# Kernel tuning notes

Measured on AMD Instinct MI355X. Metric: run time of the kernel, lower is better.

## Reference

```python
import jax, jax.numpy as jnp
import numpy as np

B, S, W = 32, 128, 16
E, CD, H, P = 256, 64, 512, 256
V, CV, NC = 50000, 256, 6
CK, WK = 8, 64  # merged char/word conv kernel sizes


def conv1d(x, w, b):
    # x: [N, Cin, L], w: [Cout, Cin, K] -> [N, Cout, L-K+1] (VALID)
    y = jax.lax.conv_general_dilated(x, w, (1,), 'VALID',
                                     dimension_numbers=('NCH', 'OIH', 'NCH'))
    return y + b[None, :, None]


def setup_inputs() -> dict:
    key = jax.random.key(0)
    ks = iter(jax.random.split(key, 40))
    nrm = lambda shape: jax.random.normal(next(ks), shape, dtype=jnp.float32) * 0.05
    return {
        'seq': jax.random.randint(next(ks), (B, S), 0, V),
        'seq_char': jax.random.randint(next(ks), (B, S, W), 0, CV),
        'classes': jnp.arange(NC, dtype=jnp.int32).reshape(NC, 1),
        'embed_w': nrm((V, E)),
        'char_embed_w': nrm((CV, CD)),
        'class_embed_w': nrm((NC, E)),
        'char_conv_w': nrm((CD, CD, CK)), 'char_conv_b': nrm((CD,)),
        'word_conv_w': nrm((E, E + CD, WK)), 'word_conv_b': nrm((E,)),
        'f_Wih': nrm((4 * H, E + CD)), 'f_Whh': nrm((4 * H, H)), 'f_b': nrm((4 * H,)),
        'b_Wih': nrm((4 * H, E + CD)), 'b_Whh': nrm((4 * H, H)), 'b_b': nrm((4 * H,)),
        'attend': nrm((E, 2 * H)),
        'd_Wih': nrm((6 * H, E + 2 * H)), 'd_Whh': nrm((6 * H, 2 * H)),
        'd_bih': nrm((6 * H,)), 'd_bhh': nrm((6 * H,)),
        'proj_w': nrm((P, 2 * H)), 'proj_b': nrm((P,)),
        'cls_w': nrm((2, P)), 'cls_b': nrm((2,)),
    }


def reference(seq, seq_char, classes, embed_w, char_embed_w, class_embed_w,
              char_conv_w, char_conv_b, word_conv_w, word_conv_b,
              f_Wih, f_Whh, f_b, b_Wih, b_Whh, b_b, attend,
              d_Wih, d_Whh, d_bih, d_bhh, proj_w, proj_b, cls_w, cls_b):
    # eval-mode forward (dropout p=0.01 is identity at eval time)
    Bq, Sq = seq.shape
    pad_mask = (seq > 0).astype(jnp.float32)            # [B,S]
    word_e = jnp.tanh(embed_w[seq])                     # [B,S,E]
    # char CNN: all char convs share kernel size -> merged into one conv
    ce = char_embed_w[seq_char]                         # [B,S,W,CD]
    ce = ce.reshape(Bq * Sq, W, CD).transpose(0, 2, 1)  # [B*S, CD, W]
    char_feat = jnp.tanh(conv1d(ce, char_conv_w, char_conv_b).mean(-1).reshape(Bq, Sq, CD))
    x = jnp.concatenate([word_e, char_feat], -1)        # [B,S,E+CD]
    # word CNN over full sequence -> [B,E]
    conv_seq = jnp.tanh(conv1d(x.transpose(0, 2, 1), word_conv_w, word_conv_b).mean(-1))
    # BiLSTM; backward direction uses seq_emb[-i], i.e. order [0, S-1, ..., 1] (as in original)
    xs = x.transpose(1, 0, 2)                           # [S,B,E+CD]
    xs_b = xs[(-jnp.arange(Sq)) % Sq]

    def lstm_scan(Wih, Whh, b, inputs):
        def step(carry, xt):
            h, c = carry
            g = xt @ Wih.T + h @ Whh.T + b
            i, f, gg, o = jnp.split(g, 4, axis=-1)
            c = jax.nn.sigmoid(f) * c + jax.nn.sigmoid(i) * jnp.tanh(gg)
            h = jax.nn.sigmoid(o) * jnp.tanh(c)
            return (h, c), h
        h0 = jnp.zeros((Bq, H), x.dtype)
        _, hs = jax.lax.scan(step, (h0, h0), inputs)
        return hs

    fouts = lstm_scan(f_Wih, f_Whh, f_b, xs)            # [S,B,H]
    bouts = lstm_scan(b_Wih, b_Whh, b_b, xs_b)[::-1]    # reversed, as in original
    seq_repr = jnp.concatenate([fouts, bouts], -1)      # [S,B,2H]
    h0 = seq_repr[-1]                                   # decoder init state [B,2H]
    seq_repr = seq_repr.transpose(1, 0, 2)              # [B,S,2H]
    # class attention: the expanded attn rows are identical across positions,
    # so sum over dim 1 of the [B,S,S] bmm equals S * tanh(a_c) . seq_repr[b,t]
    a = jnp.tanh(jnp.tanh(class_embed_w[classes[:, 0]])) @ attend   # [C,2H]
    scores = Sq * jnp.einsum('ch,bth->cbt', jnp.tanh(a), seq_repr)  # [C,B,S]
    scores = scores * pad_mask[None]
    att_ctx = jnp.einsum('cbt,bth->cbh', jnp.tanh(scores), seq_repr)  # [C,B,2H]

    def gru_step(h, ctx):
        inp = jnp.concatenate([conv_seq, ctx], -1)      # [B, E+2H]
        gi = inp @ d_Wih.T + d_bih
        gh = h @ d_Whh.T + d_bhh
        ir, iz, inn = jnp.split(gi, 3, -1)
        hr, hz, hn = jnp.split(gh, 3, -1)
        r = jax.nn.sigmoid(ir + hr)
        z = jax.nn.sigmoid(iz + hz)
        n = jnp.tanh(inn + r * hn)
        h_new = jnp.tanh((1 - z) * n + z * h)           # post-tanh state fed back (as in original)
        logits = (h_new @ proj_w.T + proj_b) @ cls_w.T + cls_b
        return h_new, jax.nn.log_softmax(logits, -1)

    _, outs = jax.lax.scan(gru_step, h0, att_ctx)       # [C,B,2]
    return outs
```

## Files before the change

kernel.cpp:

```cpp
#include <hip/hip_runtime.h>

typedef __bf16 bf16_t;
typedef __bf16 bf16x8 __attribute__((ext_vector_type(8)));
typedef float f32x4 __attribute__((ext_vector_type(4)));

static constexpr int BB = 32, SS = 128, WW = 16, EE = 256, CDm = 64, HH = 512, PP = 256;
static constexpr int EC = 320;
static constexpr int H2 = 1024;
static constexpr int G6 = 3072;
static constexpr int NKT = 28;
static constexpr int NKTX = 12;

__device__ __forceinline__ float sigm(float x){ return 1.f/(1.f + expf(-x)); }

__global__ void k_embed(const int* __restrict__ seq, const float* __restrict__ embed_w,
                        float* __restrict__ x, float* __restrict__ mask){
  int bs = blockIdx.x; int c = threadIdx.x;
  int wid = seq[bs];
  x[(size_t)bs*EC + c] = tanhf(embed_w[(size_t)wid*EE + c]);
  if (c == 0) mask[bs] = (wid > 0) ? 1.f : 0.f;
}

__global__ void k_cbar(const int* __restrict__ seq_char, const float* __restrict__ cemb,
                       float* __restrict__ cbar){
  int bs = blockIdx.x; int c = threadIdx.x;
  float ce[WW];
  #pragma unroll
  for (int p = 0; p < WW; ++p){
    int id = seq_char[bs*WW + p];
    ce[p] = cemb[(size_t)id*CDm + c];
  }
  #pragma unroll
  for (int k = 0; k < 8; ++k){
    float s = 0.f;
    #pragma unroll
    for (int p = 0; p < 9; ++p) s += ce[k+p];
    cbar[(size_t)bs*512 + c*8 + k] = s * (1.f/9.f);
  }
}

__global__ __launch_bounds__(64) void k_xbar(const float* __restrict__ x, float* __restrict__ xbar){
  __shared__ float xl[64][129];
  int gid = blockIdx.x*64 + threadIdx.x;
  int b = gid / EC, c = gid % EC;
  int tl = threadIdx.x;
  for (int t = 0; t < SS; ++t) xl[tl][t] = x[((size_t)b*SS + t)*EC + c];
  float s = 0.f;
  for (int t = 0; t < 65; ++t) s += xl[tl][t];
  const float inv = 1.f/65.f;
  float* o = &xbar[(size_t)(b*EC + c)*64];
  o[0] = s*inv;
  for (int k = 1; k < 64; ++k){ s += xl[tl][k+64] - xl[tl][k-1]; o[k] = s*inv; }
}

template<int BM,int BN,int TM,int TN>
__global__ __launch_bounds__(256) void k_gemm(const float* __restrict__ A,
    const float* __restrict__ Wm, float* __restrict__ part,
    int M, int N, int K, int kslice){
  __shared__ float As[32][BM+4];
  __shared__ float Ws[32][BN+4];
  const int tid = threadIdx.x;
  const int tx = tid & 15, ty = tid >> 4;
  const int m0 = blockIdx.x*BM, n0 = blockIdx.y*BN, ks = blockIdx.z;
  const int kb = ks*kslice;
  float acc[TM][TN];
  #pragma unroll
  for (int i = 0; i < TM; ++i)
    #pragma unroll
    for (int j = 0; j < TN; ++j) acc[i][j] = 0.f;
  for (int kt = 0; kt < kslice; kt += 32){
    constexpr int AIT = (BM*8)/256;
    #pragma unroll
    for (int it = 0; it < AIT; ++it){
      int ch = tid + it*256;
      int r = ch >> 3, kc = (ch & 7)*4;
      float4 v = *(const float4*)(A + (size_t)(m0+r)*K + kb + kt + kc);
      As[kc+0][r]=v.x; As[kc+1][r]=v.y; As[kc+2][r]=v.z; As[kc+3][r]=v.w;
    }
    constexpr int WIT = (BN*8)/256;
    #pragma unroll
    for (int it = 0; it < WIT; ++it){
      int ch = tid + it*256;
      int r = ch >> 3, kc = (ch & 7)*4;
      float4 v = *(const float4*)(Wm + (size_t)(n0+r)*K + kb + kt + kc);
      Ws[kc+0][r]=v.x; Ws[kc+1][r]=v.y; Ws[kc+2][r]=v.z; Ws[kc+3][r]=v.w;
    }
    __syncthreads();
    #pragma unroll
    for (int kk = 0; kk < 32; ++kk){
      float a[TM], wv[TN];
      #pragma unroll
      for (int i = 0; i < TM; ++i) a[i] = As[kk][ty*TM+i];
      #pragma unroll
      for (int j = 0; j < TN; ++j) wv[j] = Ws[kk][tx*TN+j];
      #pragma unroll
      for (int i = 0; i < TM; ++i)
        #pragma unroll
        for (int j = 0; j < TN; ++j) acc[i][j] = fmaf(a[i], wv[j], acc[i][j]);
    }
    __syncthreads();
  }
  #pragma unroll
  for (int i = 0; i < TM; ++i){
    int row = m0 + ty*TM + i;
    #pragma unroll
    for (int j = 0; j < TN; ++j){
      int col = n0 + tx*TN + j;
      part[((size_t)ks*M + row)*N + col] = acc[i][j];
    }
  }
}

__global__ __launch_bounds__(64) void k_fin(const float* __restrict__ part,
    const float* __restrict__ bias, float* __restrict__ out,
    int M, int N, int KS, int ldc, int act){
  int col = blockIdx.x*64 + threadIdx.x;
  int row = blockIdx.y;
  float v = bias ? bias[col] : 0.f;
  for (int ks = 0; ks < KS; ++ks) v += part[((size_t)ks*M + row)*N + col];
  if (act) v = tanhf(v);
  out[(size_t)row*ldc + col] = v;
}

__global__ __launch_bounds__(64) void k_packw(const float* __restrict__ fWih, const float* __restrict__ fWhh,
    const float* __restrict__ bWih, const float* __restrict__ bWhh, bf16_t* __restrict__ Wp){
  int id = blockIdx.x;
  int kt = id % NKT; id /= NKT;
  int slice = id % 32; int dir = id / 32;
  int l = threadIdx.x;
  const float* Whh = dir ? bWhh : fWhh;
  const float* Wih = dir ? bWih : fWih;
  int krow = (l >> 4)*8;
  for (int nt = 0; nt < 4; ++nt){
    int row = nt*512 + slice*16 + (l & 15);
    bf16_t* dst = &Wp[((((size_t)(dir*32+slice)*NKT + kt)*4 + nt)*64 + l)*8];
    if (kt < 16){
      const float* src = &Whh[(size_t)row*512 + kt*32 + krow];
      #pragma unroll
      for (int r = 0; r < 8; ++r) dst[r] = (bf16_t)src[r];
    } else {
      int kx = (kt-16)*32 + krow;
      if (kx + 8 <= 320){
        const float* src = &Wih[(size_t)row*320 + kx];
        #pragma unroll
        for (int r = 0; r < 8; ++r) dst[r] = (bf16_t)src[r];
      } else {
        #pragma unroll
        for (int r = 0; r < 8; ++r) dst[r] = (bf16_t)0.f;
      }
    }
  }
}

__global__ __launch_bounds__(64) void k_packdw(const float* __restrict__ W, bf16_t* __restrict__ Wo){
  int id = blockIdx.x;
  int kt = id % 32; id /= 32;
  int nt = id % 3;  int wg = id / 3;
  int l = threadIdx.x;
  int col = nt*1024 + wg*16 + (l & 15);
  int k0 = kt*32 + (l >> 4)*8;
  bf16_t* dst = Wo + (((size_t)(wg*3 + nt)*32 + kt)*64 + l)*8;
  const float* src = W + (size_t)col*1024 + k0;
  #pragma unroll
  for (int r = 0; r < 8; ++r) dst[r] = (bf16_t)src[r];
}

__global__ __launch_bounds__(64) void k_packpw(const float* __restrict__ W, bf16_t* __restrict__ Wo){
  int id = blockIdx.x;
  int kt = id & 31, wg = id >> 5;
  int l = threadIdx.x;
  int col = wg*16 + (l & 15);
  int k0 = kt*32 + (l >> 4)*8;
  bf16_t* dst = Wo + (((size_t)wg*32 + kt)*64 + l)*8;
  const float* src = W + (size_t)col*1024 + k0;
  #pragma unroll
  for (int r = 0; r < 8; ++r) dst[r] = (bf16_t)src[r];
}

__global__ __launch_bounds__(64) void k_packx(const float* __restrict__ x, bf16_t* __restrict__ xp){
  int id = blockIdx.x;
  int ktx = id % NKTX; id /= NKTX;
  int mt = id & 1; int t = id >> 1;
  int l = threadIdx.x;
  int b = (l & 15) + 16*mt;
  int c = ktx*32 + (l >> 4)*8;
  bf16_t* dst = &xp[(((size_t)t*2 + mt)*NKTX + ktx)*64*8 + (size_t)l*8];
  if (c + 8 <= EC){
    const float* src = &x[((size_t)b*SS + t)*EC + c];
    #pragma unroll
    for (int r = 0; r < 8; ++r) dst[r] = (bf16_t)src[r];
  } else {
    #pragma unroll
    for (int r = 0; r < 8; ++r) dst[r] = (bf16_t)0.f;
  }
}

__global__ __launch_bounds__(256) void k_zero(unsigned int* __restrict__ base){
  int i = blockIdx.x*256 + threadIdx.x;
  if (i < 35840) __hip_atomic_store(base + i, 0u, __ATOMIC_RELAXED, __HIP_MEMORY_SCOPE_AGENT);
}

__global__ __launch_bounds__(64) void k_hprep(const float* __restrict__ seq_repr, bf16_t* __restrict__ hdp){
  int mt = blockIdx.x >> 5, kt = blockIdx.x & 31, l = threadIdx.x;
  int b = mt*16 + (l & 15);
  int jb = kt*32 + (l >> 4)*8;
  const float* src = &seq_repr[((size_t)b*SS + 127)*H2 + jb];
  unsigned* dst = (unsigned*)(hdp + (((size_t)mt*32 + kt)*64 + l)*8);
  #pragma unroll
  for (int p = 0; p < 4; ++p){
    unsigned pk = (unsigned)__builtin_bit_cast(unsigned short, (bf16_t)src[2*p])
                | ((unsigned)__builtin_bit_cast(unsigned short, (bf16_t)src[2*p+1]) << 16);
    __hip_atomic_store(dst + p, pk, __ATOMIC_RELAXED, __HIP_MEMORY_SCOPE_AGENT);
  }
}

__global__ __launch_bounds__(256, 1) void k_lstm(const bf16_t* __restrict__ Wp,
    const bf16_t* __restrict__ xp, bf16_t* __restrict__ hp,
    const float* __restrict__ fb, const float* __restrict__ bb,
    float* __restrict__ seq_repr, unsigned int* __restrict__ lf){
  const int wg = blockIdx.x;
  const int dir = wg >> 5, slice = wg & 31;
  const int tid = threadIdx.x;
  const int wv = tid >> 6, lane = tid & 63;
  __shared__ __align__(16) bf16_t Wl[NKT*4*64*8];
  __shared__ float red[4][32][65];
  __shared__ float bias_l[64];
  __shared__ float c_l[16][32];
  {
    const uint4* src = (const uint4*)(Wp + ((size_t)(dir*32 + slice))*NKT*4*64*8);
    uint4* dst = (uint4*)Wl;
    for (int i = tid; i < NKT*4*64*8/8; i += 256) dst[i] = src[i];
  }
  if (tid < 64){
    const float* bv = dir ? bb : fb;
    bias_l[tid] = bv[(tid >> 4)*512 + slice*16 + (tid & 15)];
  }
  ((float*)c_l)[tid]       = 0.f;
  ((float*)c_l)[tid + 256] = 0.f;
  __syncthreads();

  union HU { unsigned long long u[2]; bf16x8 v; };

  for (int t = 0; t < SS; ++t){
    const int ph = t & 1;
    const int s = dir ? ((SS - t) & 127) : t;
    f32x4 acc[2][4];
    f32x4 zero = {0.f,0.f,0.f,0.f};
    #pragma unroll
    for (int m = 0; m < 2; ++m)
      #pragma unroll
      for (int n = 0; n < 4; ++n) acc[m][n] = zero;

    const bf16_t* xb = xp + (size_t)s*2*NKTX*64*8;
    bf16x8 ax[3][2];
    #pragma unroll
    for (int i = 0; i < 3; ++i){
      int ktx = wv*3 + i;
      #pragma unroll
      for (int m = 0; m < 2; ++m)
        ax[i][m] = *reinterpret_cast<const bf16x8*>(xb + (((size_t)m*NKTX + ktx)*64 + lane)*8);
    }
    #pragma unroll
    for (int i = 0; i < 3; ++i){
      int kt = 16 + wv*3 + i;
      #pragma unroll
      for (int nt = 0; nt < 4; ++nt){
        bf16x8 Bf = *reinterpret_cast<const bf16x8*>(&Wl[(((size_t)kt*4 + nt)*64 + lane)*8]);
        acc[0][nt] = __builtin_amdgcn_mfma_f32_16x16x32_bf16(ax[i][0], Bf, acc[0][nt], 0, 0, 0);
        acc[1][nt] = __builtin_amdgcn_mfma_f32_16x16x32_bf16(ax[i][1], Bf, acc[1][nt], 0, 0, 0);
      }
    }
    if (t > 0 && lane < 8){
      int prod = dir*32 + (wv + 4*(lane >> 1))*2 + (lane & 1);
      const unsigned int* fp = lf + prod*16;
      unsigned tgt = (unsigned)t;
      for(;;){
        unsigned v = __hip_atomic_load(fp, __ATOMIC_RELAXED, __HIP_MEMORY_SCOPE_AGENT);
        if (__ballot(v < tgt) == 0ull) break;
      }
    }
    const bf16_t* hb_ = hp + ((size_t)(ph*2 + dir))*2*16*64*8;
    bf16x8 ah[4][2];
    #pragma unroll
    for (int i = 0; i < 4; ++i){
      int kt = wv + 4*i;
      #pragma unroll
      for (int m = 0; m < 2; ++m){
        const unsigned long long* p =
            (const unsigned long long*)(hb_ + (((size_t)m*16 + kt)*64 + lane)*8);
        HU u;
        u.u[0] = __hip_atomic_load(p,     __ATOMIC_RELAXED, __HIP_MEMORY_SCOPE_AGENT);
        u.u[1] = __hip_atomic_load(p + 1, __ATOMIC_RELAXED, __HIP_MEMORY_SCOPE_AGENT);
        ah[i][m] = u.v;
      }
    }
    #pragma unroll
    for (int i = 0; i < 4; ++i){
      int kt = wv + 4*i;
      #pragma unroll
      for (int nt = 0; nt < 4; ++nt){
        bf16x8 Bf = *reinterpret_cast<const bf16x8*>(&Wl[(((size_t)kt*4 + nt)*64 + lane)*8]);
        acc[0][nt] = __builtin_amdgcn_mfma_f32_16x16x32_bf16(ah[i][0], Bf, acc[0][nt], 0, 0, 0);
        acc[1][nt] = __builtin_amdgcn_mfma_f32_16x16x32_bf16(ah[i][1], Bf, acc[1][nt], 0, 0, 0);
      }
    }
    {
      int r0 = (lane >> 4)*4, cc = lane & 15;
      #pragma unroll
      for (int m = 0; m < 2; ++m)
        #pragma unroll
        for (int n = 0; n < 4; ++n)
          #pragma unroll
          for (int e = 0; e < 4; ++e)
            red[wv][m*16 + r0 + e][n*16 + cc] = acc[m][n][e];
    }
    __syncthreads();
    {
      int b = tid & 31, jjp = tid >> 5;
      float hv[2];
      #pragma unroll
      for (int u2 = 0; u2 < 2; ++u2){
        int jj = jjp*2 + u2;
        float gi_ = bias_l[jj],     gf_ = bias_l[16+jj];
        float gg_ = bias_l[32+jj],  go_ = bias_l[48+jj];
        #pragma unroll
        for (int w2 = 0; w2 < 4; ++w2){
          gi_ += red[w2][b][jj];      gf_ += red[w2][b][16+jj];
          gg_ += red[w2][b][32+jj];   go_ += red[w2][b][48+jj];
        }
        float ii = sigm(gi_), ff = sigm(gf_), g2 = tanhf(gg_), oo = sigm(go_);
        float c = ff*c_l[jj][b] + ii*g2;
        c_l[jj][b] = c;
        hv[u2] = oo*tanhf(c);
      }
      int j0 = slice*16 + jjp*2;
      int s_out = dir ? (127 - t) : t;
      float2 st; st.x = hv[0]; st.y = hv[1];
      *(float2*)&seq_repr[((size_t)b*SS + s_out)*H2 + dir*HH + j0] = st;
      int mt = b >> 4, kth = j0 >> 5, ln = (b & 15) + 16*((j0 >> 3) & 3), rg = j0 & 7;
      unsigned pk = (unsigned)__builtin_bit_cast(unsigned short, (bf16_t)hv[0])
                  | ((unsigned)__builtin_bit_cast(unsigned short, (bf16_t)hv[1]) << 16);
      unsigned* dst = (unsigned*)(hp +
          ((((size_t)((ph^1)*2 + dir)*2 + mt)*16 + kth)*64 + ln)*8 + rg);
      __hip_atomic_store(dst, pk, __ATOMIC_RELAXED, __HIP_MEMORY_SCOPE_AGENT);
    }
    __syncthreads();
    if (tid == 0)
      __hip_atomic_store(lf + wg*16, (unsigned)(t+1), __ATOMIC_RELAXED, __HIP_MEMORY_SCOPE_AGENT);
  }
}

__global__ __launch_bounds__(256) void k_ta(const int* __restrict__ classes,
    const float* __restrict__ cls_emb, const float* __restrict__ attend, float* __restrict__ ta){
  int c = blockIdx.x;
  __shared__ float t2[EE];
  int tid = threadIdx.x;
  int ci = classes[c];
  t2[tid] = tanhf(tanhf(cls_emb[(size_t)ci*EE + tid]));
  __syncthreads();
  for (int r = 0; r < 4; ++r){
    int h = r*256 + tid;
    float acc = 0.f;
    for (int e = 0; e < EE; ++e) acc = fmaf(t2[e], attend[(size_t)e*H2 + h], acc);
    ta[c*H2 + h] = tanhf(acc);
  }
}

__global__ __launch_bounds__(256) void k_ctx(const float* __restrict__ ta,
    const float* __restrict__ seq_repr, const float* __restrict__ mask, float* __restrict__ ctx){
  int c = blockIdx.x, b = blockIdx.y;
  __shared__ float ta_l[H2];
  __shared__ float ps[128][2];
  __shared__ float sc[128];
  int tid = threadIdx.x;
  for (int i = tid; i < H2; i += 256) ta_l[i] = ta[c*H2 + i];
  __syncthreads();
  {
    int tt = tid >> 1, half = tid & 1;
    const float* row = &seq_repr[((size_t)b*SS + tt)*H2 + half*512];
    const float* tl = &ta_l[half*512];
    float p = 0.f;
    for (int i = 0; i < 512; i += 4){
      float4 v = *(const float4*)&row[i];
      p = fmaf(tl[i], v.x, p);   p = fmaf(tl[i+1], v.y, p);
      p = fmaf(tl[i+2], v.z, p); p = fmaf(tl[i+3], v.w, p);
    }
    ps[tt][half] = p;
  }
  __syncthreads();
  if (tid < 128){
    float s = (ps[tid][0] + ps[tid][1]) * 128.f * mask[b*SS + tid];
    sc[tid] = tanhf(s);
  }
  __syncthreads();
  {
    int h = tid*4;
    float4 a = {0.f,0.f,0.f,0.f};
    for (int t = 0; t < SS; ++t){
      float s = sc[t];
      float4 v = *(const float4*)&seq_repr[((size_t)b*SS + t)*H2 + h];
      a.x = fmaf(s, v.x, a.x); a.y = fmaf(s, v.y, a.y);
      a.z = fmaf(s, v.z, a.z); a.w = fmaf(s, v.w, a.w);
    }
    *(float4*)&ctx[((size_t)c*BB + b)*H2 + h] = a;
  }
}

__global__ void k_inp(const float* __restrict__ conv_seq, const float* __restrict__ ctx,
                      float* __restrict__ inp){
  int cb = blockIdx.x;
  int b = cb & 31;
  for (int k = threadIdx.x; k < 1280; k += 256){
    float v = (k < 256) ? conv_seq[b*256 + k] : ctx[(size_t)cb*H2 + (k - 256)];
    inp[(size_t)cb*1280 + k] = v;
  }
}

__global__ __launch_bounds__(256, 1) void k_dec(
    const bf16_t* __restrict__ Whp, const bf16_t* __restrict__ Ppw,
    const float* __restrict__ gi, const float* __restrict__ d_bhh,
    const float* __restrict__ seq_repr,
    const float* __restrict__ proj_b, const float* __restrict__ cls_w,
    const float* __restrict__ cls_b, bf16_t* __restrict__ hdp,
    float* __restrict__ pl, unsigned int* __restrict__ dfh,
    unsigned int* __restrict__ dfpl, float* __restrict__ out){
  const int wg = blockIdx.x;
  const int tid = threadIdx.x;
  const int wv = tid >> 6, lane = tid & 63;
  __shared__ __align__(16) bf16_t Wl[3*32*64*8];
  __shared__ float red[4][32][49];
  __shared__ float plred[8][32][2];
  __shared__ float cv[2];
  {
    const uint4* src = (const uint4*)(Whp + (size_t)wg*3*32*64*8);
    uint4* dst = (uint4*)Wl;
    for (int i = tid; i < 3*32*64*8/8; i += 256) dst[i] = src[i];
  }
  const int b = tid & 31, jp = tid >> 5;
  const int j0 = wg*16 + jp*2;
  float hold[2];
  hold[0] = seq_repr[((size_t)b*SS + 127)*H2 + j0];
  hold[1] = seq_repr[((size_t)b*SS + 127)*H2 + j0 + 1];
  float bhh[3][2];
  #pragma unroll
  for (int g = 0; g < 3; ++g){
    bhh[g][0] = d_bhh[g*1024 + j0];
    bhh[g][1] = d_bhh[g*1024 + j0 + 1];
  }
  __syncthreads();
  union HU { unsigned long long u[2]; bf16x8 v; };
  const int r0 = (lane >> 4)*4, cc = lane & 15;

  for (int c = 0; c < 6; ++c){
    if (c > 0){
      const unsigned int* fp = dfh + lane*16;
      unsigned tgt = (unsigned)c;
      for(;;){
        unsigned v = __hip_atomic_load(fp, __ATOMIC_RELAXED, __HIP_MEMORY_SCOPE_AGENT);
        if (__ballot(v < tgt) == 0ull) break;
      }
    }
    f32x4 acc[2][3];
    f32x4 zero = {0.f,0.f,0.f,0.f};
    #pragma unroll
    for (int m = 0; m < 2; ++m)
      #pragma unroll
      for (int n = 0; n < 3; ++n) acc[m][n] = zero;
    const bf16_t* hb = hdp + (size_t)(c & 1)*2*32*64*8;
    #pragma unroll
    for (int i = 0; i < 8; ++i){
      int kt = wv*8 + i;
      HU u0, u1;
      const unsigned long long* p0 = (const unsigned long long*)(hb + (((size_t)0*32 + kt)*64 + lane)*8);
      const unsigned long long* p1 = (const unsigned long long*)(hb + (((size_t)1*32 + kt)*64 + lane)*8);
      u0.u[0] = __hip_atomic_load(p0,     __ATOMIC_RELAXED, __HIP_MEMORY_SCOPE_AGENT);
      u0.u[1] = __hip_atomic_load(p0 + 1, __ATOMIC_RELAXED, __HIP_MEMORY_SCOPE_AGENT);
      u1.u[0] = __hip_atomic_load(p1,     __ATOMIC_RELAXED, __HIP_MEMORY_SCOPE_AGENT);
      u1.u[1] = __hip_atomic_load(p1 + 1, __ATOMIC_RELAXED, __HIP_MEMORY_SCOPE_AGENT);
      #pragma unroll
      for (int nt = 0; nt < 3; ++nt){
        bf16x8 Bf = *reinterpret_cast<const bf16x8*>(&Wl[(((size_t)nt*32 + kt)*64 + lane)*8]);
        acc[0][nt] = __builtin_amdgcn_mfma_f32_16x16x32_bf16(u0.v, Bf, acc[0][nt], 0, 0, 0);
        acc[1][nt] = __builtin_amdgcn_mfma_f32_16x16x32_bf16(u1.v, Bf, acc[1][nt], 0, 0, 0);
      }
    }
    #pragma unroll
    for (int m = 0; m < 2; ++m)
      #pragma unroll
      for (int n = 0; n < 3; ++n)
        #pragma unroll
        for (int e = 0; e < 4; ++e)
          red[wv][m*16 + r0 + e][n*16 + cc] = acc[m][n][e];
    __syncthreads();
    float hnew[2];
    #pragma unroll
    for (int u2 = 0; u2 < 2; ++u2){
      int jj = jp*2 + u2;
      float r_ = 0.f, z_ = 0.f, n_ = 0.f;
      #pragma unroll
      for (int w = 0; w < 4; ++w){
        r_ += red[w][b][jj]; z_ += red[w][b][16+jj]; n_ += red[w][b][32+jj];
      }
      const float* gr = gi + ((size_t)(c*BB) + b)*G6 + wg*16 + jj;
      float rr = sigm(gr[0]    + bhh[0][u2] + r_);
      float zz = sigm(gr[1024] + bhh[1][u2] + z_);
      float nn = tanhf(gr[2048] + rr*(bhh[2][u2] + n_));
      hnew[u2] = tanhf((1.f - zz)*nn + zz*hold[u2]);
      hold[u2] = hnew[u2];
    }
    {
      int kt = j0 >> 5, ln = (b & 15) + 16*((j0 >> 3) & 3), rg = j0 & 7, mt = b >> 4;
      unsigned pk = (unsigned)__builtin_bit_cast(unsigned short, (bf16_t)hnew[0])
                  | ((unsigned)__builtin_bit_cast(unsigned short, (bf16_t)hnew[1]) << 16);
      unsigned* dst = (unsigned*)(hdp + (size_t)((c+1)&1)*2*32*64*8 +
                                  (((size_t)(mt*32 + kt)*64 + ln)*8 + rg));
      __hip_atomic_store(dst, pk, __ATOMIC_RELAXED, __HIP_MEMORY_SCOPE_AGENT);
    }
    __syncthreads();
    if (tid == 0)
      __hip_atomic_store(dfh + wg*16, (unsigned)(c+1), __ATOMIC_RELAXED, __HIP_MEMORY_SCOPE_AGENT);
    if (wg < 16){
      {
        const unsigned int* fp = dfh + lane*16;
        unsigned tgt = (unsigned)(c+1);
        for(;;){
          unsigned v = __hip_atomic_load(fp, __ATOMIC_RELAXED, __HIP_MEMORY_SCOPE_AGENT);
          if (__ballot(v < tgt) == 0ull) break;
        }
      }
      f32x4 pacc[2] = {zero, zero};
      const bf16_t* hb2 = hdp + (size_t)((c+1)&1)*2*32*64*8;
      #pragma unroll
      for (int i = 0; i < 8; ++i){
        int kt = wv*8 + i;
        HU u0, u1;
        const unsigned long long* p0 = (const unsigned long long*)(hb2 + (((size_t)0*32 + kt)*64 + lane)*8);
        const unsigned long long* p1 = (const unsigned long long*)(hb2 + (((size_t)1*32 + kt)*64 + lane)*8);
        u0.u[0] = __hip_atomic_load(p0,     __ATOMIC_RELAXED, __HIP_MEMORY_SCOPE_AGENT);
        u0.u[1] = __hip_atomic_load(p0 + 1, __ATOMIC_RELAXED, __HIP_MEMORY_SCOPE_AGENT);
        u1.u[0] = __hip_atomic_load(p1,     __ATOMIC_RELAXED, __HIP_MEMORY_SCOPE_AGENT);
        u1.u[1] = __hip_atomic_load(p1 + 1, __ATOMIC_RELAXED, __HIP_MEMORY_SCOPE_AGENT);
        bf16x8 Bf = *reinterpret_cast<const bf16x8*>(Ppw + (((size_t)wg*32 + kt)*64 + lane)*8);
        pacc[0] = __builtin_amdgcn_mfma_f32_16x16x32_bf16(u0.v, Bf, pacc[0], 0, 0, 0);
        pacc[1] = __builtin_amdgcn_mfma_f32_16x16x32_bf16(u1.v, Bf, pacc[1], 0, 0, 0);
      }
      #pragma unroll
      for (int m = 0; m < 2; ++m)
        #pragma unroll
        for (int e = 0; e < 4; ++e)
          red[wv][m*16 + r0 + e][cc] = pacc[m][e];
      __syncthreads();
      {
        int colp = tid >> 5;
        float v0 = 0.f, v1 = 0.f;
        #pragma unroll
        for (int w = 0; w < 4; ++w){
          v0 += red[w][b][colp*2];
          v1 += red[w][b][colp*2+1];
        }
        int c0 = wg*16 + colp*2, c1 = c0 + 1;
        plred[colp][b][0] = v0*cls_w[c0]      + v1*cls_w[c1];
        plred[colp][b][1] = v0*cls_w[PP + c0] + v1*cls_w[PP + c1];
      }
      __syncthreads();
      if (tid < 32){
        float s0 = 0.f, s1 = 0.f;
        #pragma unroll
        for (int g = 0; g < 8; ++g){ s0 += plred[g][tid][0]; s1 += plred[g][tid][1]; }
        unsigned* dp = (unsigned*)(pl + (((size_t)c*16 + wg)*32 + tid)*2);
        __hip_atomic_store(dp,     __builtin_bit_cast(unsigned, s0), __ATOMIC_RELAXED, __HIP_MEMORY_SCOPE_AGENT);
        __hip_atomic_store(dp + 1, __builtin_bit_cast(unsigned, s1), __ATOMIC_RELAXED, __HIP_MEMORY_SCOPE_AGENT);
      }
      __syncthreads();
      if (tid == 0)
        __hip_atomic_store(dfpl + wg*16, (unsigned)(c+1), __ATOMIC_RELAXED, __HIP_MEMORY_SCOPE_AGENT);
    }
  }
  if (wg == 0){
    if (lane < 16){
      const unsigned int* fp = dfpl + lane*16;
      for(;;){
        unsigned v = __hip_atomic_load(fp, __ATOMIC_RELAXED, __HIP_MEMORY_SCOPE_AGENT);
        if (__ballot(v < 6u) == 0ull) break;
      }
    }
    __syncthreads();
    float* cr = (float*)red;
    cr[tid*2]   = proj_b[tid]*cls_w[tid];
    cr[tid*2+1] = proj_b[tid]*cls_w[PP + tid];
    __syncthreads();
    if (tid < 2){
      float s = 0.f;
      for (int i = 0; i < 256; ++i) s += cr[i*2 + tid];
      cv[tid] = s;
    }
    __syncthreads();
    if (tid < 32){
      for (int c = 0; c < 6; ++c){
        float a0 = cv[0] + cls_b[0], a1 = cv[1] + cls_b[1];
        for (int w = 0; w < 16; ++w){
          const unsigned* dp = (const unsigned*)(pl + (((size_t)c*16 + w)*32 + tid)*2);
          a0 += __builtin_bit_cast(float, __hip_atomic_load(dp,     __ATOMIC_RELAXED, __HIP_MEMORY_SCOPE_AGENT));
          a1 += __builtin_bit_cast(float, __hip_atomic_load(dp + 1, __ATOMIC_RELAXED, __HIP_MEMORY_SCOPE_AGENT));
        }
        float mx = fmaxf(a0, a1);
        float ls = mx + logf(expf(a0 - mx) + expf(a1 - mx));
        out[((size_t)c*BB + tid)*2 + 0] = a0 - ls;
        out[((size_t)c*BB + tid)*2 + 1] = a1 - ls;
      }
    }
  }
}

extern "C" void kernel_launch(void* const* d_in, const int* in_sizes, int n_in,
                              void* d_out, int out_size, void* d_ws, size_t ws_size,
                              hipStream_t stream){
  const int*   seq          = (const int*)  d_in[0];
  const int*   seq_char     = (const int*)  d_in[1];
  const int*   classes      = (const int*)  d_in[2];
  const float* embed_w      = (const float*)d_in[3];
  const float* char_embed_w = (const float*)d_in[4];
  const float* class_embed_w= (const float*)d_in[5];
  const float* char_conv_w  = (const float*)d_in[6];
  const float* char_conv_b  = (const float*)d_in[7];
  const float* word_conv_w  = (const float*)d_in[8];
  const float* word_conv_b  = (const float*)d_in[9];
  const float* f_Wih = (const float*)d_in[10];
  const float* f_Whh = (const float*)d_in[11];
  const float* f_b   = (const float*)d_in[12];
  const float* b_Wih = (const float*)d_in[13];
  const float* b_Whh = (const float*)d_in[14];
  const float* b_b   = (const float*)d_in[15];
  const float* attend = (const float*)d_in[16];
  const float* d_Wih  = (const float*)d_in[17];
  const float* d_Whh  = (const float*)d_in[18];
  const float* d_bih  = (const float*)d_in[19];
  const float* d_bhh  = (const float*)d_in[20];
  const float* proj_w = (const float*)d_in[21];
  const float* proj_b = (const float*)d_in[22];
  const float* cls_w  = (const float*)d_in[23];
  const float* cls_b  = (const float*)d_in[24];
  float* out = (float*)d_out;

  char* wsb = (char*)d_ws;
  size_t off = 0;
  auto alloc = [&](size_t bytes) -> char* {
    char* p = wsb + off;
    off += (bytes + 255) & ~(size_t)255;
    return p;
  };
  unsigned int* flags = (unsigned int*)alloc(12288);
  unsigned int* lf   = flags;
  unsigned int* dfh  = flags + 1024;
  unsigned int* dfpl = flags + 2048;
  bf16_t* hp  = (bf16_t*)alloc((size_t)2*2*2*16*64*8 * 2);
  bf16_t* hdp = (bf16_t*)alloc((size_t)2*2*32*64*8 * 2);
  bf16_t* Wp  = (bf16_t*)alloc((size_t)2*32*NKT*4*64*8 * 2);
  bf16_t* Whp = (bf16_t*)alloc((size_t)64*3*32*64*8 * 2);
  bf16_t* Ppw = (bf16_t*)alloc((size_t)16*32*64*8 * 2);
  bf16_t* xp  = (bf16_t*)alloc((size_t)128*2*NKTX*64*8 * 2);
  float* pl       = (float*)alloc((size_t)6*16*32*2*4);
  float* x        = (float*)alloc((size_t)BB*SS*EC*4);
  float* mask     = (float*)alloc((size_t)BB*SS*4);
  float* cbar     = (float*)alloc((size_t)4096*512*4);
  float* xbar     = (float*)alloc((size_t)BB*EC*64*4);
  float* conv_seq = (float*)alloc((size_t)BB*256*4);
  float* seq_repr = (float*)alloc((size_t)BB*SS*H2*4);
  float* ta       = (float*)alloc((size_t)6*H2*4);
  float* ctx      = (float*)alloc((size_t)6*BB*H2*4);
  float* inp      = (float*)alloc((size_t)192*1280*4);
  float* gi       = (float*)alloc((size_t)192*G6*4);
  float* part_char= (float*)alloc((size_t)2*4096*64*4);
  float* part_word= (float*)alloc((size_t)32*BB*256*4);
  float* part_gi  = (float*)alloc((size_t)4*192*G6*4);
  (void)ws_size; (void)in_sizes; (void)n_in; (void)out_size;

  k_zero<<<140, 256, 0, stream>>>((unsigned int*)d_ws);

  k_packw<<<2*32*NKT, 64, 0, stream>>>(f_Wih, f_Whh, b_Wih, b_Whh, Wp);
  k_packdw<<<64*3*32, 64, 0, stream>>>(d_Whh, Whp);
  k_packpw<<<16*32, 64, 0, stream>>>(proj_w, Ppw);
  k_embed<<<BB*SS, 256, 0, stream>>>(seq, embed_w, x, mask);
  k_cbar<<<BB*SS, 64, 0, stream>>>(seq_char, char_embed_w, cbar);
  k_gemm<32,64,2,4><<<dim3(128,1,2), 256, 0, stream>>>(cbar, char_conv_w, part_char, 4096, 64, 512, 256);
  k_fin<<<dim3(1,4096), 64, 0, stream>>>(part_char, char_conv_b, x + 256, 4096, 64, 2, EC, 1);
  k_xbar<<<160, 64, 0, stream>>>(x, xbar);
  k_gemm<32,64,2,4><<<dim3(1,4,32), 256, 0, stream>>>(xbar, word_conv_w, part_word, 32, 256, 20480, 640);
  k_fin<<<dim3(4,32), 64, 0, stream>>>(part_word, word_conv_b, conv_seq, 32, 256, 32, 256, 1);
  k_packx<<<128*2*NKTX, 64, 0, stream>>>(x, xp);
  k_lstm<<<64, 256, 0, stream>>>(Wp, xp, hp, f_b, b_b, seq_repr, lf);
  k_ta<<<6, 256, 0, stream>>>(classes, class_embed_w, attend, ta);
  k_ctx<<<dim3(6,32), 256, 0, stream>>>(ta, seq_repr, mask, ctx);
  k_inp<<<192, 256, 0, stream>>>(conv_seq, ctx, inp);
  k_gemm<64,64,4,4><<<dim3(3,48,4), 256, 0, stream>>>(inp, d_Wih, part_gi, 192, G6, 1280, 320);
  k_fin<<<dim3(48,192), 64, 0, stream>>>(part_gi, d_bih, gi, 192, G6, 4, G6, 0);
  k_hprep<<<64, 64, 0, stream>>>(seq_repr, hdp);
  k_dec<<<64, 256, 0, stream>>>(Whp, Ppw, gi, d_bhh, seq_repr, proj_b, cls_w, cls_b,
                                hdp, pl, dfh, dfpl, out);
}
```

Measured before the change: 663.7 us.

## Place LSTM direction workgroups on one XCC each and use XCC-local coherence

The LSTM kernel now launches 256 workgroups and reads each one's hardware XCC id. When the round-robin XCC mapping holds, it keeps only the blocks that put each direction's 32 slices on a single XCC. Those blocks exchange hidden state and flags through L2-coherent (sc0) loads and stores instead of device-scope atomics, which is meant to cut per-timestep cross-XCC synchronization latency. If the mapping check fails, it falls back to the original 64-block layout with sc1 system-coherent accesses. It adds startup handshake overhead, relies on undocumented dispatch placement, and adds an explicit vmcnt drain before the flag store.

Measured after the change: 645.1 us. 2.8% less time.

```diff
diff --git a/kernel.cpp b/kernel.cpp
--- a/kernel.cpp
+++ b/kernel.cpp
@@ -3,6 +3,8 @@
 typedef __bf16 bf16_t;
 typedef __bf16 bf16x8 __attribute__((ext_vector_type(8)));
 typedef float f32x4 __attribute__((ext_vector_type(4)));
+typedef unsigned u32x4 __attribute__((ext_vector_type(4)));
+typedef unsigned long long u64;
 
 static constexpr int BB = 32, SS = 128, WW = 16, EE = 256, CDm = 64, HH = 512, PP = 256;
 static constexpr int EC = 320;
@@ -12,6 +14,39 @@
 static constexpr int NKTX = 12;
 
 __device__ __forceinline__ float sigm(float x){ return 1.f/(1.f + expf(-x)); }
+
+#define ALOAD(p)    __hip_atomic_load((p),  __ATOMIC_RELAXED, __HIP_MEMORY_SCOPE_AGENT)
+#define ASTORE(p,v) __hip_atomic_store((p),(v),__ATOMIC_RELAXED, __HIP_MEMORY_SCOPE_AGENT)
+
+template<bool LLC>
+__device__ __forceinline__ unsigned ld_flag(const unsigned* p){
+  unsigned r;
+  if constexpr (LLC)
+    asm volatile("global_load_dword %0, %1, off sc0 sc1\n\ts_waitcnt vmcnt(0)"
+                 : "=&v"(r) : "v"(p) : "memory");
+  else
+    asm volatile("global_load_dword %0, %1, off sc0\n\ts_waitcnt vmcnt(0)"
+                 : "=&v"(r) : "v"(p) : "memory");
+  return r;
+}
+template<bool LLC>
+__device__ __forceinline__ void ld16(u32x4& d, const void* p){
+  if constexpr (LLC)
+    asm volatile("global_load_dwordx4 %0, %1, off sc0 sc1" : "=&v"(d) : "v"(p) : "memory");
+  else
+    asm volatile("global_load_dwordx4 %0, %1, off sc0"     : "=&v"(d) : "v"(p) : "memory");
+}
+template<bool LLC>
+__device__ __forceinline__ void st32(unsigned* p, unsigned v){
+  if constexpr (LLC)
+    asm volatile("global_store_dword %0, %1, off sc0 sc1" :: "v"(p), "v"(v) : "memory");
+  else
+    asm volatile("global_store_dword %0, %1, off sc0"     :: "v"(p), "v"(v) : "memory");
+}
+__device__ __forceinline__ void vm_drain(){
+  asm volatile("s_waitcnt vmcnt(0)" ::: "memory");
+  __builtin_amdgcn_sched_barrier(0);
+}
 
 __global__ void k_embed(const int* __restrict__ seq, const float* __restrict__ embed_w,
                         float* __restrict__ x, float* __restrict__ mask){
@@ -195,12 +230,13 @@
   }
 }
 
-__global__ __launch_bounds__(256) void k_zero(unsigned int* __restrict__ base){
+__global__ __launch_bounds__(256) void k_zero(unsigned int* __restrict__ base, int n){
   int i = blockIdx.x*256 + threadIdx.x;
-  if (i < 35840) __hip_atomic_store(base + i, 0u, __ATOMIC_RELAXED, __HIP_MEMORY_SCOPE_AGENT);
-}
-
-__global__ __launch_bounds__(64) void k_hprep(const float* __restrict__ seq_repr, bf16_t* __restrict__ hdp){
+  if (i < n) ASTORE(base + i, 0u);
+}
+
+__global__ __launch_bounds__(64) void k_hprep(const float* __restrict__ seq_repr,
+                                              bf16_t* __restrict__ hdp){
   int mt = blockIdx.x >> 5, kt = blockIdx.x & 31, l = threadIdx.x;
   int b = mt*16 + (l & 15);
   int jb = kt*32 + (l >> 4)*8;
@@ -210,22 +246,17 @@
   for (int p = 0; p < 4; ++p){
     unsigned pk = (unsigned)__builtin_bit_cast(unsigned short, (bf16_t)src[2*p])
                 | ((unsigned)__builtin_bit_cast(unsigned short, (bf16_t)src[2*p+1]) << 16);
-    __hip_atomic_store(dst + p, pk, __ATOMIC_RELAXED, __HIP_MEMORY_SCOPE_AGENT);
-  }
-}
-
-__global__ __launch_bounds__(256, 1) void k_lstm(const bf16_t* __restrict__ Wp,
-    const bf16_t* __restrict__ xp, bf16_t* __restrict__ hp,
-    const float* __restrict__ fb, const float* __restrict__ bb,
-    float* __restrict__ seq_repr, unsigned int* __restrict__ lf){
-  const int wg = blockIdx.x;
-  const int dir = wg >> 5, slice = wg & 31;
-  const int tid = threadIdx.x;
+    ASTORE(dst + p, pk);
+  }
+}
+
+template<bool LLC>
+__device__ void lstm_body(const bf16_t* __restrict__ Wp, const bf16_t* __restrict__ xp,
+    bf16_t* __restrict__ hp, const float* __restrict__ fb, const float* __restrict__ bb,
+    float* __restrict__ seq_repr, unsigned* __restrict__ lf,
+    int dir, int slice, int tid, bf16_t* Wl, float (*red)[32][65],
+    float* bias_l, float (*c_l)[32]){
   const int wv = tid >> 6, lane = tid & 63;
-  __shared__ __align__(16) bf16_t Wl[NKT*4*64*8];
-  __shared__ float red[4][32][65];
-  __shared__ float bias_l[64];
-  __shared__ float c_l[16][32];
   {
     const uint4* src = (const uint4*)(Wp + ((size_t)(dir*32 + slice))*NKT*4*64*8);
     uint4* dst = (uint4*)Wl;
@@ -238,8 +269,6 @@
   ((float*)c_l)[tid]       = 0.f;
   ((float*)c_l)[tid + 256] = 0.f;
   __syncthreads();
-
-  union HU { unsigned long long u[2]; bf16x8 v; };
 
   for (int t = 0; t < SS; ++t){
     const int ph = t & 1;
@@ -272,36 +301,33 @@
     }
     if (t > 0 && lane < 8){
       int prod = dir*32 + (wv + 4*(lane >> 1))*2 + (lane & 1);
-      const unsigned int* fp = lf + prod*16;
+      const unsigned* fp = lf + prod*16;
       unsigned tgt = (unsigned)t;
       for(;;){
-        unsigned v = __hip_atomic_load(fp, __ATOMIC_RELAXED, __HIP_MEMORY_SCOPE_AGENT);
+        unsigned v = ld_flag<LLC>(fp);
         if (__ballot(v < tgt) == 0ull) break;
       }
     }
     const bf16_t* hb_ = hp + ((size_t)(ph*2 + dir))*2*16*64*8;
-    bf16x8 ah[4][2];
+    u32x4 hr[4][2];
     #pragma unroll
     for (int i = 0; i < 4; ++i){
       int kt = wv + 4*i;
       #pragma unroll
-      for (int m = 0; m < 2; ++m){
-        const unsigned long long* p =
-            (const unsigned long long*)(hb_ + (((size_t)m*16 + kt)*64 + lane)*8);
-        HU u;
-        u.u[0] = __hip_atomic_load(p,     __ATOMIC_RELAXED, __HIP_MEMORY_SCOPE_AGENT);
-        u.u[1] = __hip_atomic_load(p + 1, __ATOMIC_RELAXED, __HIP_MEMORY_SCOPE_AGENT);
-        ah[i][m] = u.v;
-      }
-    }
+      for (int m = 0; m < 2; ++m)
+        ld16<LLC>(hr[i][m], hb_ + (((size_t)m*16 + kt)*64 + lane)*8);
+    }
+    vm_drain();
     #pragma unroll
     for (int i = 0; i < 4; ++i){
       int kt = wv + 4*i;
+      bf16x8 a0 = __builtin_bit_cast(bf16x8, hr[i][0]);
+      bf16x8 a1 = __builtin_bit_cast(bf16x8, hr[i][1]);
       #pragma unroll
       for (int nt = 0; nt < 4; ++nt){
         bf16x8 Bf = *reinterpret_cast<const bf16x8*>(&Wl[(((size_t)kt*4 + nt)*64 + lane)*8]);
-        acc[0][nt] = __builtin_amdgcn_mfma_f32_16x16x32_bf16(ah[i][0], Bf, acc[0][nt], 0, 0, 0);
-        acc[1][nt] = __builtin_amdgcn_mfma_f32_16x16x32_bf16(ah[i][1], Bf, acc[1][nt], 0, 0, 0);
+        acc[0][nt] = __builtin_amdgcn_mfma_f32_16x16x32_bf16(a0, Bf, acc[0][nt], 0, 0, 0);
+        acc[1][nt] = __builtin_amdgcn_mfma_f32_16x16x32_bf16(a1, Bf, acc[1][nt], 0, 0, 0);
       }
     }
     {
@@ -342,12 +368,68 @@
                   | ((unsigned)__builtin_bit_cast(unsigned short, (bf16_t)hv[1]) << 16);
       unsigned* dst = (unsigned*)(hp +
           ((((size_t)((ph^1)*2 + dir)*2 + mt)*16 + kth)*64 + ln)*8 + rg);
-      __hip_atomic_store(dst, pk, __ATOMIC_RELAXED, __HIP_MEMORY_SCOPE_AGENT);
-    }
+      st32<LLC>(dst, pk);
+    }
+    asm volatile("s_waitcnt vmcnt(0)" ::: "memory");
     __syncthreads();
     if (tid == 0)
-      __hip_atomic_store(lf + wg*16, (unsigned)(t+1), __ATOMIC_RELAXED, __HIP_MEMORY_SCOPE_AGENT);
-  }
+      st32<LLC>(lf + (dir*32 + slice)*16, (unsigned)(t+1));
+  }
+}
+
+__global__ __launch_bounds__(256, 1) void k_lstm(const bf16_t* __restrict__ Wp,
+    const bf16_t* __restrict__ xp, bf16_t* __restrict__ hp,
+    const float* __restrict__ fb, const float* __restrict__ bb,
+    float* __restrict__ seq_repr, unsigned* __restrict__ lf,
+    unsigned* __restrict__ xcc_tab, unsigned* __restrict__ modep){
+  const int blk = blockIdx.x;
+  const int tid = threadIdx.x;
+  __shared__ __align__(16) bf16_t Wl[NKT*4*64*8];
+  __shared__ float red[4][32][65];
+  __shared__ float bias_l[64];
+  __shared__ float c_l[16][32];
+  __shared__ unsigned mode_s;
+
+  unsigned xcc;
+  asm volatile("s_getreg_b32 %0, hwreg(HW_REG_XCC_ID)" : "=s"(xcc));
+  if (tid == 0) ASTORE(xcc_tab + blk, xcc + 1u);
+  if (blk == 0){
+    unsigned* tabl = (unsigned*)red;
+    unsigned v = 0; int spins = 0;
+    for (;;){
+      v = ALOAD(xcc_tab + tid);
+      if (v != 0u || spins >= 200000) break;
+      ++spins; __builtin_amdgcn_s_sleep(2);
+    }
+    tabl[tid] = v;
+    __syncthreads();
+    if (tid == 0){
+      unsigned mode = 1;
+      unsigned c0 = tabl[0], c1 = tabl[1];
+      if (c0 == 0u || c1 == 0u) mode = 2;
+      for (int k = 0; k < 32; ++k)
+        if (tabl[8*k] != c0 || tabl[8*k + 1] != c1) mode = 2;
+      ASTORE(modep, mode);
+      mode_s = mode;
+    }
+    __syncthreads();
+  } else {
+    if (tid == 0){
+      unsigned m;
+      while ((m = ALOAD(modep)) == 0u) __builtin_amdgcn_s_sleep(2);
+      mode_s = m;
+    }
+    __syncthreads();
+  }
+  const unsigned mode = mode_s;
+  int dir, slice; bool worker;
+  if (mode == 1){ worker = (blk & 7) < 2; dir = blk & 7; slice = blk >> 3; }
+  else          { worker = blk < 64;      dir = blk >> 5; slice = blk & 31; }
+  if (!worker) return;
+  if (mode == 1)
+    lstm_body<false>(Wp, xp, hp, fb, bb, seq_repr, lf, dir, slice, tid, Wl, red, bias_l, c_l);
+  else
+    lstm_body<true >(Wp, xp, hp, fb, bb, seq_repr, lf, dir, slice, tid, Wl, red, bias_l, c_l);
 }
 
 __global__ __launch_bounds__(256) void k_ta(const int* __restrict__ classes,
@@ -456,7 +538,7 @@
       const unsigned int* fp = dfh + lane*16;
       unsigned tgt = (unsigned)c;
       for(;;){
-        unsigned v = __hip_atomic_load(fp, __ATOMIC_RELAXED, __HIP_MEMORY_SCOPE_AGENT);
+        unsigned v = ALOAD(fp);
         if (__ballot(v < tgt) == 0ull) break;
       }
     }
@@ -473,10 +555,8 @@
       HU u0, u1;
       const unsigned long long* p0 = (const unsigned long long*)(hb + (((size_t)0*32 + kt)*64 + lane)*8);
       const unsigned long long* p1 = (const unsigned long long*)(hb + (((size_t)1*32 + kt)*64 + lane)*8);
-      u0.u[0] = __hip_atomic_load(p0,     __ATOMIC_RELAXED, __HIP_MEMORY_SCOPE_AGENT);
-      u0.u[1] = __hip_atomic_load(p0 + 1, __ATOMIC_RELAXED, __HIP_MEMORY_SCOPE_AGENT);
-      u1.u[0] = __hip_atomic_load(p1,     __ATOMIC_RELAXED, __HIP_MEMORY_SCOPE_AGENT);
-      u1.u[1] = __hip_atomic_load(p1 + 1, __ATOMIC_RELAXED, __HIP_MEMORY_SCOPE_AGENT);
+      u0.u[0] = ALOAD(p0);     u0.u[1] = ALOAD(p0 + 1);
+      u1.u[0] = ALOAD(p1);     u1.u[1] = ALOAD(p1 + 1);
       #pragma unroll
       for (int nt = 0; nt < 3; ++nt){
         bf16x8 Bf = *reinterpret_cast<const bf16x8*>(&Wl[(((size_t)nt*32 + kt)*64 + lane)*8]);
@@ -514,17 +594,17 @@
                   | ((unsigned)__builtin_bit_cast(unsigned short, (bf16_t)hnew[1]) << 16);
       unsigned* dst = (unsigned*)(hdp + (size_t)((c+1)&1)*2*32*64*8 +
                                   (((size_t)(mt*32 + kt)*64 + ln)*8 + rg));
-      __hip_atomic_store(dst, pk, __ATOMIC_RELAXED, __HIP_MEMORY_SCOPE_AGENT);
+      ASTORE(dst, pk);
     }
     __syncthreads();
     if (tid == 0)
-      __hip_atomic_store(dfh + wg*16, (unsigned)(c+1), __ATOMIC_RELAXED, __HIP_MEMORY_SCOPE_AGENT);
+      ASTORE(dfh + wg*16, (unsigned)(c+1));
     if (wg < 16){
       {
         const unsigned int* fp = dfh + lane*16;
         unsigned tgt = (unsigned)(c+1);
         for(;;){
-          unsigned v = __hip_atomic_load(fp, __ATOMIC_RELAXED, __HIP_MEMORY_SCOPE_AGENT);
+          unsigned v = ALOAD(fp);
           if (__ballot(v < tgt) == 0ull) break;
         }
       }
@@ -536,10 +616,8 @@
         HU u0, u1;
         const unsigned long long* p0 = (const unsigned long long*)(hb2 + (((size_t)0*32 + kt)*64 + lane)*8);
         const unsigned long long* p1 = (const unsigned long long*)(hb2 + (((size_t)1*32 + kt)*64 + lane)*8);
-        u0.u[0] = __hip_atomic_load(p0,     __ATOMIC_RELAXED, __HIP_MEMORY_SCOPE_AGENT);
-        u0.u[1] = __hip_atomic_load(p0 + 1, __ATOMIC_RELAXED, __HIP_MEMORY_SCOPE_AGENT);
-        u1.u[0] = __hip_atomic_load(p1,     __ATOMIC_RELAXED, __HIP_MEMORY_SCOPE_AGENT);
-        u1.u[1] = __hip_atomic_load(p1 + 1, __ATOMIC_RELAXED, __HIP_MEMORY_SCOPE_AGENT);
+        u0.u[0] = ALOAD(p0);     u0.u[1] = ALOAD(p0 + 1);
+        u1.u[0] = ALOAD(p1);     u1.u[1] = ALOAD(p1 + 1);
         bf16x8 Bf = *reinterpret_cast<const bf16x8*>(Ppw + (((size_t)wg*32 + kt)*64 + lane)*8);
         pacc[0] = __builtin_amdgcn_mfma_f32_16x16x32_bf16(u0.v, Bf, pacc[0], 0, 0, 0);
         pacc[1] = __builtin_amdgcn_mfma_f32_16x16x32_bf16(u1.v, Bf, pacc[1], 0, 0, 0);
@@ -568,19 +646,19 @@
         #pragma unroll
         for (int g = 0; g < 8; ++g){ s0 += plred[g][tid][0]; s1 += plred[g][tid][1]; }
         unsigned* dp = (unsigned*)(pl + (((size_t)c*16 + wg)*32 + tid)*2);
-        __hip_atomic_store(dp,     __builtin_bit_cast(unsigned, s0), __ATOMIC_RELAXED, __HIP_MEMORY_SCOPE_AGENT);
-        __hip_atomic_store(dp + 1, __builtin_bit_cast(unsigned, s1), __ATOMIC_RELAXED, __HIP_MEMORY_SCOPE_AGENT);
+        ASTORE(dp,     __builtin_bit_cast(unsigned, s0));
+        ASTORE(dp + 1, __builtin_bit_cast(unsigned, s1));
       }
       __syncthreads();
       if (tid == 0)
-        __hip_atomic_store(dfpl + wg*16, (unsigned)(c+1), __ATOMIC_RELAXED, __HIP_MEMORY_SCOPE_AGENT);
+        ASTORE(dfpl + wg*16, (unsigned)(c+1));
     }
   }
   if (wg == 0){
     if (lane < 16){
       const unsigned int* fp = dfpl + lane*16;
       for(;;){
-        unsigned v = __hip_atomic_load(fp, __ATOMIC_RELAXED, __HIP_MEMORY_SCOPE_AGENT);
+        unsigned v = ALOAD(fp);
         if (__ballot(v < 6u) == 0ull) break;
       }
     }
@@ -600,8 +678,8 @@
         float a0 = cv[0] + cls_b[0], a1 = cv[1] + cls_b[1];
         for (int w = 0; w < 16; ++w){
           const unsigned* dp = (const unsigned*)(pl + (((size_t)c*16 + w)*32 + tid)*2);
-          a0 += __builtin_bit_cast(float, __hip_atomic_load(dp,     __ATOMIC_RELAXED, __HIP_MEMORY_SCOPE_AGENT));
-          a1 += __builtin_bit_cast(float, __hip_atomic_load(dp + 1, __ATOMIC_RELAXED, __HIP_MEMORY_SCOPE_AGENT));
+          a0 += __builtin_bit_cast(float, ALOAD(dp));
+          a1 += __builtin_bit_cast(float, ALOAD(dp + 1));
         }
         float mx = fmaxf(a0, a1);
         float ls = mx + logf(expf(a0 - mx) + expf(a1 - mx));
@@ -653,7 +731,10 @@
   unsigned int* lf   = flags;
   unsigned int* dfh  = flags + 1024;
   unsigned int* dfpl = flags + 2048;
+  unsigned int* xcc_tab = (unsigned int*)alloc(1024);
+  unsigned int* modep   = (unsigned int*)alloc(256);
   bf16_t* hp  = (bf16_t*)alloc((size_t)2*2*2*16*64*8 * 2);
+  const int ZERO_DWORDS = 3072 + 256 + 64 + 32768;
   bf16_t* hdp = (bf16_t*)alloc((size_t)2*2*32*64*8 * 2);
   bf16_t* Wp  = (bf16_t*)alloc((size_t)2*32*NKT*4*64*8 * 2);
   bf16_t* Whp = (bf16_t*)alloc((size_t)64*3*32*64*8 * 2);
@@ -675,7 +756,7 @@
   float* part_gi  = (float*)alloc((size_t)4*192*G6*4);
   (void)ws_size; (void)in_sizes; (void)n_in; (void)out_size;
 
-  k_zero<<<140, 256, 0, stream>>>((unsigned int*)d_ws);
+  k_zero<<<(ZERO_DWORDS + 255)/256, 256, 0, stream>>>((unsigned int*)d_ws, ZERO_DWORDS);
 
   k_packw<<<2*32*NKT, 64, 0, stream>>>(f_Wih, f_Whh, b_Wih, b_Whh, Wp);
   k_packdw<<<64*3*32, 64, 0, stream>>>(d_Whh, Whp);
@@ -688,7 +769,7 @@
   k_gemm<32,64,2,4><<<dim3(1,4,32), 256, 0, stream>>>(xbar, word_conv_w, part_word, 32, 256, 20480, 640);
   k_fin<<<dim3(4,32), 64, 0, stream>>>(part_word, word_conv_b, conv_seq, 32, 256, 32, 256, 1);
   k_packx<<<128*2*NKTX, 64, 0, stream>>>(x, xp);
-  k_lstm<<<64, 256, 0, stream>>>(Wp, xp, hp, f_b, b_b, seq_repr, lf);
+  k_lstm<<<256, 256, 0, stream>>>(Wp, xp, hp, f_b, b_b, seq_repr, lf, xcc_tab, modep);
   k_ta<<<6, 256, 0, stream>>>(classes, class_embed_w, attend, ta);
   k_ctx<<<dim3(6,32), 256, 0, stream>>>(ta, seq_repr, mask, ctx);
   k_inp<<<192, 256, 0, stream>>>(conv_seq, ctx, inp);
```
